# Optimization experiments

Hardware: AMD Instinct MI355X
Metric: run time of the kernel (lower is better)

The kernel has to match this reference:

```python
import jax, jax.numpy as jnp
import numpy as np

B, T, D, H, O = 32768, 96, 7, 3, 7

def setup_inputs() -> dict:
    key = jax.random.key(0)
    ks = jax.random.split(key, 7)
    s_ih = 1.0 / np.sqrt(H)
    inp = {
        "x": jax.random.normal(ks[0], (B, T, D), dtype=jnp.float32),
        # PyTorch nn.LSTM params (gate order i,f,g,o), uniform(-1/sqrt(H), 1/sqrt(H))
        "W_ih": jax.random.uniform(ks[1], (4 * H, D), jnp.float32, -s_ih, s_ih),
        "W_hh": jax.random.uniform(ks[2], (4 * H, H), jnp.float32, -s_ih, s_ih),
        "b_ih": jax.random.uniform(ks[3], (4 * H,), jnp.float32, -s_ih, s_ih),
        "b_hh": jax.random.uniform(ks[4], (4 * H,), jnp.float32, -s_ih, s_ih),
        # nn.Linear(H*T, O*T): weight [out,in]
        "W_lin": jax.random.uniform(ks[5], (O * T, H * T), jnp.float32, -1.0 / np.sqrt(H * T), 1.0 / np.sqrt(H * T)),
        "b_lin": jax.random.uniform(ks[6], (O * T,), jnp.float32, -1.0 / np.sqrt(H * T), 1.0 / np.sqrt(H * T)),
    }
    return inp

def _lstm(x, W_ih, W_hh, b_ih, b_hh):
    b = x.shape[0]
    h0 = jnp.zeros((b, H), x.dtype)
    c0 = jnp.zeros((b, H), x.dtype)
    bias = b_ih + b_hh

    def step(carry, x_t):
        h, c = carry
        gates = x_t @ W_ih.T + h @ W_hh.T + bias  # [b, 4H]
        i, f, g, o = jnp.split(gates, 4, axis=-1)
        i = jax.nn.sigmoid(i)
        f = jax.nn.sigmoid(f)
        g = jnp.tanh(g)
        o = jax.nn.sigmoid(o)
        c = f * c + i * g
        h = o * jnp.tanh(c)
        return (h, c), h

    (_, _), hs = jax.lax.scan(step, (h0, c0), jnp.swapaxes(x, 0, 1))  # hs: [T, b, H]
    return jnp.swapaxes(hs, 0, 1)  # [b, T, H]

def reference(x, W_ih, W_hh, b_ih, b_hh, W_lin, b_lin):
    out = _lstm(x, W_ih, W_hh, b_ih, b_hh)            # [B, T, H]
    out = out.reshape(x.shape[0], -1)                  # [B, T*H]
    out = out @ W_lin.T + b_lin                        # [B, O*T]
    return out.reshape(x.shape)                        # [B, T, D]
```

## Files before the change

kernel.cpp:

```cpp
#include <hip/hip_runtime.h>
#include <stdint.h>

typedef unsigned short u16;
typedef unsigned int u32;
typedef __attribute__((ext_vector_type(8))) __bf16 bf16x8;
typedef __attribute__((ext_vector_type(4))) float f32x4;

#define B_TOT   32768
#define T_SEQ   96
#define D_IN    7
#define K_LIN   288
#define N_LIN   672
#define N_PAD   768

__device__ __forceinline__ u16 f2bf(float f) {
  u32 u = __builtin_bit_cast(u32, f);
  u += 0x7fffu + ((u >> 16) & 1u);
  return (u16)(u >> 16);
}
__device__ __forceinline__ float fast_sig(float z) {
  return __builtin_amdgcn_rcpf(1.0f + __expf(-z));
}
__device__ __forceinline__ float fast_tanh(float z) {
  return 1.0f - 2.0f * __builtin_amdgcn_rcpf(1.0f + __expf(2.0f * z));
}

__global__ __launch_bounds__(256) void convert_kernel(
    const float* __restrict__ Wlin, const float* __restrict__ blin,
    u16* __restrict__ Bw, float* __restrict__ biasp)
{
  int i = blockIdx.x * 256 + threadIdx.x;
  if (i < N_PAD * K_LIN) {
    int n = i / K_LIN;
    Bw[i] = f2bf((n < N_LIN) ? Wlin[i] : 0.0f);
  }
  if (i < N_PAD) biasp[i] = (i < N_LIN) ? blin[i] : 0.0f;
}

__device__ __forceinline__ void lstm_step(
    const float* xt, float* h, float* c,
    const float (&wih)[12][7], const float (&whh)[12][3], const float (&bias)[12],
    u16* pk)
{
  float z[12];
#pragma unroll
  for (int g = 0; g < 12; ++g) {
    float a = bias[g];
#pragma unroll
    for (int k = 0; k < 7; ++k) a = fmaf(xt[k], wih[g][k], a);
#pragma unroll
    for (int j = 0; j < 3; ++j) a = fmaf(h[j], whh[g][j], a);
    z[g] = a;
  }
#pragma unroll
  for (int j = 0; j < 3; ++j) {
    float ig = fast_sig(z[j]);
    float fg = fast_sig(z[3 + j]);
    float gg = fast_tanh(z[6 + j]);
    float og = fast_sig(z[9 + j]);
    float cn = fmaf(fg, c[j], ig * gg);
    c[j] = cn;
    float hv = og * fast_tanh(cn);
    h[j] = hv;
    pk[j] = f2bf(hv);
  }
}

__global__ __launch_bounds__(64) void lstm_kernel(
    const float* __restrict__ x,
    const float* __restrict__ Wih, const float* __restrict__ Whh,
    const float* __restrict__ bih, const float* __restrict__ bhh,
    u16* __restrict__ hs)
{
  __shared__ float sW[132];
  const int tid = threadIdx.x;
  for (int i = tid; i < 132; i += 64) {
    float v;
    if (i < 84)       v = Wih[i];
    else if (i < 120) v = Whh[i - 84];
    else              v = bih[i - 120] + bhh[i - 120];
    sW[i] = v;
  }
  __syncthreads();

  float wih[12][7], whh[12][3], bias[12];
#pragma unroll
  for (int g = 0; g < 12; ++g) {
#pragma unroll
    for (int k = 0; k < 7; ++k) wih[g][k] = sW[g * 7 + k];
#pragma unroll
    for (int j = 0; j < 3; ++j) whh[g][j] = sW[84 + g * 3 + j];
    bias[g] = sW[120 + g];
  }

  const int b = blockIdx.x * 64 + tid;
  const float4* __restrict__ xr = (const float4*)(x + (size_t)b * (T_SEQ * D_IN));
  u16* __restrict__ hrow = hs + (size_t)b * K_LIN;

  float h[3] = {0.f, 0.f, 0.f};
  float c[3] = {0.f, 0.f, 0.f};
  float xa[28] __attribute__((aligned(16)));
  float xb[28] __attribute__((aligned(16)));
  u16 pk[24] __attribute__((aligned(16)));

#pragma unroll
  for (int q = 0; q < 7; ++q) ((float4*)xa)[q] = xr[q];

#pragma unroll 1
  for (int g8 = 0; g8 < 12; ++g8) {
#pragma unroll
    for (int q = 0; q < 7; ++q) ((float4*)xb)[q] = xr[(2 * g8 + 1) * 7 + q];
#pragma unroll
    for (int s = 0; s < 4; ++s)
      lstm_step(xa + s * 7, h, c, wih, whh, bias, pk + s * 3);
    if (g8 < 11) {
#pragma unroll
      for (int q = 0; q < 7; ++q) ((float4*)xa)[q] = xr[(2 * g8 + 2) * 7 + q];
    }
#pragma unroll
    for (int s = 0; s < 4; ++s)
      lstm_step(xb + s * 7, h, c, wih, whh, bias, pk + 12 + s * 3);
    uint4* dst = (uint4*)(hrow + g8 * 24);
    const uint4* src = (const uint4*)pk;
    dst[0] = src[0]; dst[1] = src[1]; dst[2] = src[2];
  }
}

__device__ __forceinline__ void gload16(const u16* g, u16* l) {
  __builtin_amdgcn_global_load_lds(
      (const __attribute__((address_space(1))) void*)g,
      (__attribute__((address_space(3))) void*)l, 16, 0, 0);
}

__global__ __launch_bounds__(256) void gemm_kernel(
    const u16* __restrict__ A, const u16* __restrict__ Bw,
    const float* __restrict__ bias, float* __restrict__ C)
{
  __shared__ u16 As[128 * 32];
  __shared__ u16 Bs[128 * 32];
  const int tid  = threadIdx.x;
  const int lane = tid & 63;
  const int wid  = tid >> 6;
  const int wm = wid >> 1, wn = wid & 1;

  int bx = blockIdx.x;
  int swz = (bx & 7) * 192 + (bx >> 3);
  const int bm = swz / 6;
  const int bn = swz - bm * 6;
  const size_t m0 = (size_t)bm * 128;
  const int n0 = bn * 128;

  const int ra = tid >> 2;
  const int ca = (tid & 3) * 8;
  const u16* ga = A  + (m0 + (size_t)ra) * K_LIN + ca;
  const u16* gb = Bw + (size_t)(n0 + ra) * K_LIN + ca;
  u16* lA = &As[wid * 512];
  u16* lB = &Bs[wid * 512];

  const int l15 = lane & 15, l4 = lane >> 4;
  const u16* pAf = &As[(wm * 64 + l15) * 32 + l4 * 8];
  const u16* pBf = &Bs[(wn * 64 + l15) * 32 + l4 * 8];

  f32x4 acc[4][4] = {};

  for (int kt = 0; kt < 9; ++kt) {
    const int ko = kt * 32;
    gload16(ga + ko,               lA);
    gload16(ga + 64 * K_LIN + ko,  lA + 2048);
    gload16(gb + ko,               lB);
    gload16(gb + 64 * K_LIN + ko,  lB + 2048);
    __syncthreads();
    bf16x8 af[4], bfv[4];
#pragma unroll
    for (int i = 0; i < 4; ++i) af[i]  = *(const bf16x8*)(const void*)(pAf + i * 512);
#pragma unroll
    for (int i = 0; i < 4; ++i) bfv[i] = *(const bf16x8*)(const void*)(pBf + i * 512);
#pragma unroll
    for (int mi = 0; mi < 4; ++mi)
#pragma unroll
      for (int ni = 0; ni < 4; ++ni)
        acc[mi][ni] = __builtin_amdgcn_mfma_f32_16x16x32_bf16(af[mi], bfv[ni], acc[mi][ni], 0, 0, 0);
    __syncthreads();
  }

  float bv[4];
#pragma unroll
  for (int ni = 0; ni < 4; ++ni) bv[ni] = bias[n0 + wn * 64 + ni * 16 + l15];

#pragma unroll
  for (int mi = 0; mi < 4; ++mi) {
#pragma unroll
    for (int ni = 0; ni < 4; ++ni) {
      const int col = n0 + wn * 64 + ni * 16 + l15;
      if (col < N_LIN) {
#pragma unroll
        for (int r = 0; r < 4; ++r) {
          const size_t row = m0 + wm * 64 + mi * 16 + l4 * 4 + r;
          C[row * N_LIN + col] = acc[mi][ni][r] + bv[ni];
        }
      }
    }
  }
}

extern "C" void kernel_launch(void* const* d_in, const int* in_sizes, int n_in,
                              void* d_out, int out_size, void* d_ws, size_t ws_size,
                              hipStream_t stream) {
  const float* x    = (const float*)d_in[0];
  const float* Wih  = (const float*)d_in[1];
  const float* Whh  = (const float*)d_in[2];
  const float* bih  = (const float*)d_in[3];
  const float* bhh  = (const float*)d_in[4];
  const float* Wlin = (const float*)d_in[5];
  const float* blin = (const float*)d_in[6];
  float* out = (float*)d_out;

  u16* hs = (u16*)d_ws;
  u16* Bw = (u16*)((char*)d_ws + (size_t)B_TOT * K_LIN * 2);
  float* biasp = (float*)((char*)d_ws + (size_t)B_TOT * K_LIN * 2 + (size_t)N_PAD * K_LIN * 2);

  convert_kernel<<<(N_PAD * K_LIN + 255) / 256, 256, 0, stream>>>(Wlin, blin, Bw, biasp);
  lstm_kernel<<<B_TOT / 64, 64, 0, stream>>>(x, Wih, Whh, bih, bhh, hs);
  gemm_kernel<<<(B_TOT / 128) * (N_PAD / 128), 256, 0, stream>>>(hs, Bw, biasp, out);
}
```

Measured before the change: 83.44 us.

## Split LSTM hidden units across four lanes with DPP broadcast of h

The LSTM kernel now assigns each batch row to four lanes, each computing the gates for one hidden unit, and shares the new h values between the lanes through DPP quad broadcasts. The hidden-state workspace layout becomes unit-major (j*96+t), and the weight conversion permutes W_lin's K dimension to match. The aim is four times more threads on the serial recurrence, which shortens the per-thread dependency chain and raises occupancy. In exchange, every lane loads the full x row redundantly, and the fourth lane of each quad does duplicate work.

```diff
diff --git a/kernel.cpp b/kernel.cpp
--- a/kernel.cpp
+++ b/kernel.cpp
@@ -24,6 +24,12 @@
 __device__ __forceinline__ float fast_tanh(float z) {
   return 1.0f - 2.0f * __builtin_amdgcn_rcpf(1.0f + __expf(2.0f * z));
 }
+template<int Q>
+__device__ __forceinline__ float qbcast(float v) {
+  int i = __builtin_bit_cast(int, v);
+  i = __builtin_amdgcn_update_dpp(0, i, Q * 0x55, 0xF, 0xF, true);
+  return __builtin_bit_cast(float, i);
+}
 
 __global__ __launch_bounds__(256) void convert_kernel(
     const float* __restrict__ Wlin, const float* __restrict__ blin,
@@ -32,41 +38,51 @@
   int i = blockIdx.x * 256 + threadIdx.x;
   if (i < N_PAD * K_LIN) {
     int n = i / K_LIN;
-    Bw[i] = f2bf((n < N_LIN) ? Wlin[i] : 0.0f);
+    int kk = i - n * K_LIN;
+    int jm = kk / T_SEQ;
+    int tm = kk - jm * T_SEQ;
+    Bw[i] = f2bf((n < N_LIN) ? Wlin[n * K_LIN + tm * 3 + jm] : 0.0f);
   }
   if (i < N_PAD) biasp[i] = (i < N_LIN) ? blin[i] : 0.0f;
 }
 
-__device__ __forceinline__ void lstm_step(
-    const float* xt, float* h, float* c,
-    const float (&wih)[12][7], const float (&whh)[12][3], const float (&bias)[12],
+__device__ __forceinline__ void chunk4(
+    const float* xc,
+    float& h0, float& h1, float& h2, float& c,
+    const float (&wih)[4][7], const float (&whh)[4][3], const float (&bias)[4],
     u16* pk)
 {
-  float z[12];
-#pragma unroll
-  for (int g = 0; g < 12; ++g) {
-    float a = bias[g];
-#pragma unroll
-    for (int k = 0; k < 7; ++k) a = fmaf(xt[k], wih[g][k], a);
-#pragma unroll
-    for (int j = 0; j < 3; ++j) a = fmaf(h[j], whh[g][j], a);
-    z[g] = a;
-  }
-#pragma unroll
-  for (int j = 0; j < 3; ++j) {
-    float ig = fast_sig(z[j]);
-    float fg = fast_sig(z[3 + j]);
-    float gg = fast_tanh(z[6 + j]);
-    float og = fast_sig(z[9 + j]);
-    float cn = fmaf(fg, c[j], ig * gg);
-    c[j] = cn;
-    float hv = og * fast_tanh(cn);
-    h[j] = hv;
-    pk[j] = f2bf(hv);
-  }
-}
-
-__global__ __launch_bounds__(64) void lstm_kernel(
+  float zx[4][4];
+#pragma unroll
+  for (int s = 0; s < 4; ++s) {
+#pragma unroll
+    for (int G = 0; G < 4; ++G) {
+      float a = bias[G];
+#pragma unroll
+      for (int k = 0; k < 7; ++k) a = fmaf(xc[s * 7 + k], wih[G][k], a);
+      zx[s][G] = a;
+    }
+  }
+#pragma unroll
+  for (int s = 0; s < 4; ++s) {
+    float zi = fmaf(h2, whh[0][2], fmaf(h1, whh[0][1], fmaf(h0, whh[0][0], zx[s][0])));
+    float zf = fmaf(h2, whh[1][2], fmaf(h1, whh[1][1], fmaf(h0, whh[1][0], zx[s][1])));
+    float zg = fmaf(h2, whh[2][2], fmaf(h1, whh[2][1], fmaf(h0, whh[2][0], zx[s][2])));
+    float zo = fmaf(h2, whh[3][2], fmaf(h1, whh[3][1], fmaf(h0, whh[3][0], zx[s][3])));
+    float ig = fast_sig(zi);
+    float fg = fast_sig(zf);
+    float gg = fast_tanh(zg);
+    float og = fast_sig(zo);
+    c = fmaf(fg, c, ig * gg);
+    float hv = og * fast_tanh(c);
+    pk[s] = f2bf(hv);
+    h0 = qbcast<0>(hv);
+    h1 = qbcast<1>(hv);
+    h2 = qbcast<2>(hv);
+  }
+}
+
+__global__ __launch_bounds__(256) void lstm_kernel(
     const float* __restrict__ x,
     const float* __restrict__ Wih, const float* __restrict__ Whh,
     const float* __restrict__ bih, const float* __restrict__ bhh,
@@ -74,7 +90,7 @@
 {
   __shared__ float sW[132];
   const int tid = threadIdx.x;
-  for (int i = tid; i < 132; i += 64) {
+  for (int i = tid; i < 132; i += 256) {
     float v;
     if (i < 84)       v = Wih[i];
     else if (i < 120) v = Whh[i - 84];
@@ -83,25 +99,28 @@
   }
   __syncthreads();
 
-  float wih[12][7], whh[12][3], bias[12];
-#pragma unroll
-  for (int g = 0; g < 12; ++g) {
-#pragma unroll
-    for (int k = 0; k < 7; ++k) wih[g][k] = sW[g * 7 + k];
-#pragma unroll
-    for (int j = 0; j < 3; ++j) whh[g][j] = sW[84 + g * 3 + j];
-    bias[g] = sW[120 + g];
-  }
-
-  const int b = blockIdx.x * 64 + tid;
+  const int j  = tid & 3;
+  const int jj = (j < 3) ? j : 2;
+
+  float wih[4][7], whh[4][3], bias[4];
+#pragma unroll
+  for (int G = 0; G < 4; ++G) {
+    const int row = G * 3 + jj;
+#pragma unroll
+    for (int k = 0; k < 7; ++k) wih[G][k] = sW[row * 7 + k];
+#pragma unroll
+    for (int m = 0; m < 3; ++m) whh[G][m] = sW[84 + row * 3 + m];
+    bias[G] = sW[120 + row];
+  }
+
+  const int b = (blockIdx.x * 256 + tid) >> 2;
   const float4* __restrict__ xr = (const float4*)(x + (size_t)b * (T_SEQ * D_IN));
-  u16* __restrict__ hrow = hs + (size_t)b * K_LIN;
-
-  float h[3] = {0.f, 0.f, 0.f};
-  float c[3] = {0.f, 0.f, 0.f};
+  u16* __restrict__ hrow = hs + (size_t)b * K_LIN + jj * T_SEQ;
+
+  float h0 = 0.f, h1 = 0.f, h2 = 0.f, c = 0.f;
   float xa[28] __attribute__((aligned(16)));
   float xb[28] __attribute__((aligned(16)));
-  u16 pk[24] __attribute__((aligned(16)));
+  u16 pk[8] __attribute__((aligned(16)));
 
 #pragma unroll
   for (int q = 0; q < 7; ++q) ((float4*)xa)[q] = xr[q];
@@ -110,19 +129,15 @@
   for (int g8 = 0; g8 < 12; ++g8) {
 #pragma unroll
     for (int q = 0; q < 7; ++q) ((float4*)xb)[q] = xr[(2 * g8 + 1) * 7 + q];
-#pragma unroll
-    for (int s = 0; s < 4; ++s)
-      lstm_step(xa + s * 7, h, c, wih, whh, bias, pk + s * 3);
+    chunk4(xa, h0, h1, h2, c, wih, whh, bias, pk);
     if (g8 < 11) {
 #pragma unroll
       for (int q = 0; q < 7; ++q) ((float4*)xa)[q] = xr[(2 * g8 + 2) * 7 + q];
     }
-#pragma unroll
-    for (int s = 0; s < 4; ++s)
-      lstm_step(xb + s * 7, h, c, wih, whh, bias, pk + 12 + s * 3);
-    uint4* dst = (uint4*)(hrow + g8 * 24);
-    const uint4* src = (const uint4*)pk;
-    dst[0] = src[0]; dst[1] = src[1]; dst[2] = src[2];
+    chunk4(xb, h0, h1, h2, c, wih, whh, bias, pk + 4);
+    if (j < 3) {
+      *(uint4*)(hrow + g8 * 8) = *(const uint4*)pk;
+    }
   }
 }
 
@@ -220,6 +235,6 @@
   float* biasp = (float*)((char*)d_ws + (size_t)B_TOT * K_LIN * 2 + (size_t)N_PAD * K_LIN * 2);
 
   convert_kernel<<<(N_PAD * K_LIN + 255) / 256, 256, 0, stream>>>(Wlin, blin, Bw, biasp);
-  lstm_kernel<<<B_TOT / 64, 64, 0, stream>>>(x, Wih, Whh, bih, bhh, hs);
+  lstm_kernel<<<(B_TOT * 4) / 256, 256, 0, stream>>>(x, Wih, Whh, bih, bhh, hs);
   gemm_kernel<<<(B_TOT / 128) * (N_PAD / 128), 256, 0, stream>>>(hs, Bw, biasp, out);
 }
```

Result: faster. 70.80 us (-15.1%).
